# Performance work log

Hardware: AMD Instinct MI355X
Metric: run time of the kernel (lower is better)

The kernel has to match this reference:

```python
import jax, jax.numpy as jnp
import numpy as np

B, S, E, H = 2, 2048, 1024, 16
D = E // H  # head_dim = 64


def setup_inputs() -> dict:
    key = jax.random.key(0)
    ks = jax.random.split(key, 9)
    sc = 1.0 / np.sqrt(E)
    return {
        "x": jax.random.normal(ks[0], (B, S, E), dtype=jnp.float32),
        "Wq": jax.random.normal(ks[1], (E, E), dtype=jnp.float32) * sc,
        "bq": jnp.zeros((E,), dtype=jnp.float32),
        "Wk": jax.random.normal(ks[2], (E, E), dtype=jnp.float32) * sc,
        "bk": jnp.zeros((E,), dtype=jnp.float32),
        "Wv": jax.random.normal(ks[3], (E, E), dtype=jnp.float32) * sc,
        "bv": jnp.zeros((E,), dtype=jnp.float32),
        "Wo": jax.random.normal(ks[4], (E, E), dtype=jnp.float32) * sc,
        "bo": jnp.zeros((E,), dtype=jnp.float32),
    }


def reference(x, Wq, bq, Wk, bk, Wv, bv, Wo, bo):
    b, s, e = x.shape
    # projections: [B,S,E] -> [B,H,S,D]
    def heads(w, bias):
        return (x @ w + bias).reshape(b, s, H, D).transpose(0, 2, 1, 3)
    q, k, v = heads(Wq, bq), heads(Wk, bk), heads(Wv, bv)
    # scores [B,H,S,S]
    scores = jnp.einsum("bhqd,bhkd->bhqk", q, k) / jnp.sqrt(jnp.float32(D))
    causal = jnp.tril(jnp.ones((s, s), dtype=bool))
    scores = jnp.where(causal[None, None], scores, -jnp.inf)
    weights = jax.nn.softmax(scores, axis=-1)
    out = jnp.einsum("bhqk,bhkd->bhqd", weights, v)
    out = out.transpose(0, 2, 1, 3).reshape(b, s, e)
    return out @ Wo + bo
```

## Files before the change

kernel.cpp:

```cpp
#include <hip/hip_runtime.h>
#include <hip/hip_bf16.h>

#define B_SZ 2
#define S_LEN 2048
#define E_DIM 1024
#define NH 16
#define DH 64
#define M_ROWS (B_SZ * S_LEN)
#define QB 128
#define KVB 64

typedef __attribute__((ext_vector_type(8))) short short8;
typedef __attribute__((ext_vector_type(4))) float floatx4;

static __device__ __forceinline__ unsigned short f2bf(float f) {
    __hip_bfloat16 h = __float2bfloat16(f);
    return *reinterpret_cast<unsigned short*>(&h);
}
static __device__ __forceinline__ float bf2f(unsigned short u) {
    unsigned int v = ((unsigned int)u) << 16;
    return __builtin_bit_cast(float, v);
}

static __device__ __forceinline__ void gl2lds16(const void* g, void* l) {
    __builtin_amdgcn_global_load_lds((const __attribute__((address_space(1))) void*)g,
                                     (__attribute__((address_space(3))) void*)l, 16, 0, 0);
}

#define WAIT_VM0() asm volatile("s_waitcnt vmcnt(0)" ::: "memory")
#define WAIT_LGKM0() asm volatile("s_waitcnt lgkmcnt(0)" ::: "memory")

__global__ __launch_bounds__(256) void prep(const float* __restrict__ x,
                                            unsigned short* __restrict__ Xb,
                                            const float* __restrict__ W0,
                                            const float* __restrict__ W1,
                                            const float* __restrict__ W2,
                                            const float* __restrict__ W3,
                                            unsigned short* __restrict__ T0,
                                            unsigned short* __restrict__ T1,
                                            unsigned short* __restrict__ T2,
                                            unsigned short* __restrict__ T3) {
    __shared__ float tile[32][33];
    int bid = blockIdx.x;
    int t = threadIdx.x;
    if (bid < 4096) {
        int i = (bid * 256 + t) * 4;
        float4 v = *reinterpret_cast<const float4*>(x + i);
        ushort4 o;
        o.x = f2bf(v.x); o.y = f2bf(v.y); o.z = f2bf(v.z); o.w = f2bf(v.w);
        *reinterpret_cast<ushort4*>(Xb + i) = o;
        return;
    }
    int u = bid - 4096;
    int z = u >> 10, rest = u & 1023;
    int bx = (rest & 31) * 32, by = (rest >> 5) * 32;
    const float* W = (z == 0) ? W0 : (z == 1) ? W1 : (z == 2) ? W2 : W3;
    unsigned short* Wt = (z == 0) ? T0 : (z == 1) ? T1 : (z == 2) ? T2 : T3;
    int tx = t & 31, ty = t >> 5;
#pragma unroll
    for (int i = 0; i < 32; i += 8)
        tile[ty + i][tx] = W[(size_t)(by + ty + i) * E_DIM + bx + tx];
    __syncthreads();
#pragma unroll
    for (int i = 0; i < 32; i += 8)
        Wt[(size_t)(bx + ty + i) * E_DIM + by + tx] = f2bf(tile[tx][ty + i]);
}

#define QSCALE 0.18033688011112042f

__global__ __launch_bounds__(512, 2) void gemm_qkv8(const unsigned short* __restrict__ Wcat,
                                                    const unsigned short* __restrict__ Xb,
                                                    const float* __restrict__ bq,
                                                    const float* __restrict__ bk,
                                                    const float* __restrict__ bv,
                                                    unsigned short* __restrict__ Qg,
                                                    unsigned short* __restrict__ Kg,
                                                    unsigned short* __restrict__ Vtg) {
    __shared__ __align__(16) char lds[2][2][32768];

    int t = threadIdx.x;
    int b = blockIdx.x;
    int xcd = b & 7, ii = b >> 3;
    int it = (xcd & 3) * 3 + (ii >> 3);
    int jt = (xcd >> 2) * 8 + (ii & 7);
    int iBase = it << 8, jBase = jt << 8;

    int w = t >> 6, lane = t & 63;
    int lr = lane & 15, lh = lane >> 4;
    int wm = w >> 2, wn = w & 3;

    int srow = t >> 3;
    int scbx = ((t & 7) << 4) ^ ((srow & 7) << 4);

    const char* Ab = (const char*)Wcat;
    const char* Bb = (const char*)Xb;

    floatx4 acc[8][4];
#pragma unroll
    for (int i = 0; i < 8; i++)
#pragma unroll
        for (int j = 0; j < 4; j++) acc[i][j] = (floatx4){0.f, 0.f, 0.f, 0.f};

    auto stageA = [&](int buf, int kt) {
        int k0b = kt << 7;
#pragma unroll
        for (int c = 0; c < 4; c++)
            gl2lds16(Ab + (size_t)(iBase + c * 64 + srow) * 2048 + k0b + scbx,
                     &lds[buf][0][c * 8192 + t * 16]);
    };
    auto stageB = [&](int buf, int kt) {
        int k0b = kt << 7;
#pragma unroll
        for (int c = 0; c < 4; c++)
            gl2lds16(Bb + (size_t)(jBase + c * 64 + srow) * 2048 + k0b + scbx,
                     &lds[buf][1][c * 8192 + t * 16]);
    };

    short8 af[4][2], bf[4][2];
    auto rdA = [&](int buf, int qm) {
#pragma unroll
        for (int mi = 0; mi < 4; mi++)
#pragma unroll
            for (int ks = 0; ks < 2; ks++) {
                int row = wm * 128 + qm * 64 + mi * 16 + lr;
                af[mi][ks] = *reinterpret_cast<const short8*>(
                    &lds[buf][0][(row * 128 + ks * 64 + lh * 16) ^ ((row & 7) << 4)]);
            }
    };
    auto rdB = [&](int buf, int qn) {
#pragma unroll
        for (int ni = 0; ni < 2; ni++)
#pragma unroll
            for (int ks = 0; ks < 2; ks++) {
                int row = wn * 64 + qn * 32 + ni * 16 + lr;
                bf[qn * 2 + ni][ks] = *reinterpret_cast<const short8*>(
                    &lds[buf][1][(row * 128 + ks * 64 + lh * 16) ^ ((row & 7) << 4)]);
            }
    };
    auto mfma16 = [&](int qm, int qn) {
        __builtin_amdgcn_s_setprio(1);
#pragma unroll
        for (int mi = 0; mi < 4; mi++)
#pragma unroll
            for (int ni = 0; ni < 2; ni++)
#pragma unroll
                for (int ks = 0; ks < 2; ks++)
                    acc[qm * 4 + mi][qn * 2 + ni] = __builtin_amdgcn_mfma_f32_16x16x32_bf16(
                        af[mi][ks], bf[qn * 2 + ni][ks], acc[qm * 4 + mi][qn * 2 + ni], 0, 0, 0);
        __builtin_amdgcn_s_setprio(0);
    };

    const int NT = 16;
    stageA(0, 0);
    stageB(0, 0);
    WAIT_VM0();
    __builtin_amdgcn_s_barrier();

    for (int kt = 0; kt < NT; ++kt) {
        int cur = kt & 1, nxt = cur ^ 1;
        bool pf = (kt + 1 < NT);
        rdA(cur, 0);
        rdB(cur, 0);
        if (pf) stageA(nxt, kt + 1);
        __builtin_amdgcn_s_barrier();
        WAIT_LGKM0();
        __builtin_amdgcn_sched_barrier(0);
        mfma16(0, 0);
        __builtin_amdgcn_s_barrier();
        rdB(cur, 1);
        if (pf) stageB(nxt, kt + 1);
        __builtin_amdgcn_s_barrier();
        WAIT_LGKM0();
        __builtin_amdgcn_sched_barrier(0);
        mfma16(0, 1);
        __builtin_amdgcn_s_barrier();
        rdA(cur, 1);
        __builtin_amdgcn_s_barrier();
        WAIT_LGKM0();
        __builtin_amdgcn_sched_barrier(0);
        mfma16(1, 0);
        __builtin_amdgcn_s_barrier();
        if (pf) WAIT_VM0();
        __builtin_amdgcn_s_barrier();
        mfma16(1, 1);
        __builtin_amdgcn_s_barrier();
    }

    int wsel = iBase >> 10;
    const float* bias = (wsel == 0) ? bq : (wsel == 1) ? bk : bv;
    __syncthreads();

    if (wsel < 2) {
        unsigned short* O = wsel ? Kg : Qg;
        float scale = wsel ? 1.0f : QSCALE;
#pragma unroll
        for (int mi8 = 0; mi8 < 8; mi8++) {
            int i = iBase + wm * 128 + mi8 * 16 + lh * 4;
            int im = i & 1023;
            int h = im >> 6, d0 = im & 63;
            float4 bs = *reinterpret_cast<const float4*>(&bias[im]);
#pragma unroll
            for (int nf = 0; nf < 4; nf++) {
                int j = jBase + wn * 64 + nf * 16 + lr;
                int b_ = j >> 11, s = j & (S_LEN - 1);
                ushort4 pk;
                pk.x = f2bf((acc[mi8][nf][0] + bs.x) * scale);
                pk.y = f2bf((acc[mi8][nf][1] + bs.y) * scale);
                pk.z = f2bf((acc[mi8][nf][2] + bs.z) * scale);
                pk.w = f2bf((acc[mi8][nf][3] + bs.w) * scale);
                *reinterpret_cast<ushort4*>(
                    &O[((size_t)(b_ * NH + h) * S_LEN + s) * DH + d0]) = pk;
            }
        }
    } else {
        char* lw = &lds[0][0][0] + w * 16384;
#pragma unroll
        for (int mi8 = 0; mi8 < 8; mi8++) {
            int i = iBase + wm * 128 + mi8 * 16 + lh * 4;
            float4 bs = *reinterpret_cast<const float4*>(&bias[i & 1023]);
#pragma unroll
            for (int nf = 0; nf < 4; nf++) {
                int jl = nf * 16 + lr;
#pragma unroll
                for (int r = 0; r < 4; r++) {
                    int il = mi8 * 16 + lh * 4 + r;
                    float bb = (r == 0) ? bs.x : (r == 1) ? bs.y : (r == 2) ? bs.z : bs.w;
                    *reinterpret_cast<unsigned short*>(
                        lw + ((il * 128 + jl * 2) ^ ((il & 7) << 4))) =
                        f2bf(acc[mi8][nf][r] + bb);
                }
            }
        }
        __syncthreads();
#pragma unroll
        for (int rep = 0; rep < 16; rep++) {
            int idx = rep * 64 + lane;
            int il = idx >> 3, jb = idx & 7;
            short8 vv = *reinterpret_cast<const short8*>(
                lw + ((il * 128 + jb * 16) ^ ((il & 7) << 4)));
            int i = iBase + wm * 128 + il;
            int im = i & 1023;
            int h = im >> 6, d = im & 63;
            int j = jBase + wn * 64 + jb * 8;
            int b_ = j >> 11, s = j & (S_LEN - 1);
            *reinterpret_cast<short8*>(
                &Vtg[((size_t)(b_ * NH + h) * DH + d) * S_LEN + s]) = vv;
        }
    }
}

template <int NI>
static __device__ __forceinline__ void gemm_tile_mainloop(
    const unsigned short* __restrict__ A, const unsigned short* __restrict__ Bt,
    int mBase, int nBase, char* ldsA, char* ldsB, floatx4 (&acc)[4][NI]) {
    const int K = E_DIM;
    int t = threadIdx.x;
    int w = t >> 6, lane = t & 63;
    int lr = lane & 15, lh = lane >> 4;
    int wm = w >> 1, wn = w & 1;
    const char* Ab = (const char*)A;
    const char* Bb = (const char*)Bt;
    int srow = t >> 3;
    int scb = ((t & 7) << 4) ^ ((srow & 7) << 4);

#pragma unroll
    for (int mi = 0; mi < 4; mi++)
#pragma unroll
        for (int ni = 0; ni < NI; ni++) acc[mi][ni] = (floatx4){0.f, 0.f, 0.f, 0.f};

    for (int kt = 0; kt < K / 64; ++kt) {
        int k0 = kt * 64;
#pragma unroll
        for (int i = 0; i < 4; i++)
            gl2lds16(Ab + (size_t)(mBase + i * 32 + srow) * (K * 2) + k0 * 2 + scb,
                     ldsA + i * 4096 + t * 16);
#pragma unroll
        for (int i = 0; i < NI; i++)
            gl2lds16(Bb + (size_t)(nBase + i * 32 + srow) * (K * 2) + k0 * 2 + scb,
                     ldsB + i * 4096 + t * 16);
        __syncthreads();
#pragma unroll
        for (int ks = 0; ks < 2; ks++) {
            short8 af[4], bfr[NI];
#pragma unroll
            for (int mi = 0; mi < 4; mi++) {
                int row = wm * 64 + mi * 16 + lr;
                af[mi] = *reinterpret_cast<const short8*>(
                    ldsA + ((row * 128 + ks * 64 + lh * 16) ^ ((row & 7) << 4)));
            }
#pragma unroll
            for (int ni = 0; ni < NI; ni++) {
                int row = wn * (NI * 16) + ni * 16 + lr;
                bfr[ni] = *reinterpret_cast<const short8*>(
                    ldsB + ((row * 128 + ks * 64 + lh * 16) ^ ((row & 7) << 4)));
            }
#pragma unroll
            for (int mi = 0; mi < 4; mi++)
#pragma unroll
                for (int ni = 0; ni < NI; ni++)
                    acc[mi][ni] = __builtin_amdgcn_mfma_f32_16x16x32_bf16(af[mi], bfr[ni],
                                                                          acc[mi][ni], 0, 0, 0);
        }
        __syncthreads();
    }
}

__global__ __launch_bounds__(256) void gemm_o(const unsigned short* __restrict__ Og,
                                              const unsigned short* __restrict__ Wot,
                                              const float* __restrict__ bo,
                                              float* __restrict__ out) {
    __shared__ __align__(16) char ldsA[16384];
    __shared__ __align__(16) char ldsB[8192];
    int bid = blockIdx.y * 16 + blockIdx.x;
    int xcd = bid & 7, ii = bid >> 3;
    int xx = ii & 15;
    int yy = (xcd << 2) | (ii >> 4);
    int nBase = xx << 6;
    int mBase = yy << 7;

    floatx4 acc[4][2];
    gemm_tile_mainloop<2>(Og, Wot, mBase, nBase, ldsA, ldsB, acc);

    int w = threadIdx.x >> 6, lane = threadIdx.x & 63;
    int lr = lane & 15, lh = lane >> 4;
    int wm = w >> 1, wn = w & 1;
#pragma unroll
    for (int mi = 0; mi < 4; mi++)
#pragma unroll
        for (int ni = 0; ni < 2; ni++)
#pragma unroll
            for (int r = 0; r < 4; r++) {
                int m = mBase + wm * 64 + mi * 16 + lh * 4 + r;
                int n = nBase + wn * 32 + ni * 16 + lr;
                out[(size_t)m * E_DIM + n] = acc[mi][ni][r] + bo[n];
            }
}

__global__ __launch_bounds__(256) void attn_fwd(const unsigned short* __restrict__ Qg,
                                                const unsigned short* __restrict__ Kg,
                                                const unsigned short* __restrict__ Vtg,
                                                unsigned short* __restrict__ Og,
                                                unsigned short* __restrict__ Opart,
                                                float* __restrict__ lpart) {
    __shared__ __align__(16) char kt_lds[2][KVB * 128];
    __shared__ __align__(16) char vt_lds[2][KVB * 128];
    __shared__ __align__(16) unsigned short p_lds[4][32][72];

    int bid = blockIdx.x;
    int xcd = bid & 7, ii = bid >> 3;
    int bh = (xcd << 2) + ii / 30;
    int jj = 29 - (ii % 30);
    int qb, ch, c;
    if (jj < 6)        { qb = jj; ch = 0; c = 1; }
    else if (jj < 18)  { int u = jj - 6;  qb = 6 + (u >> 1); ch = u & 1; c = 2; }
    else               { int u = jj - 18; qb = 12 + u / 3;   ch = u % 3; c = 3; }
    int T = 2 * qb + 2;
    int kt_lo = ch * T / c;
    int kt_hi = (ch + 1) * T / c - 1;
    bool split = (c > 1);

    int w = threadIdx.x >> 6, lane = threadIdx.x & 63;
    int lr = lane & 15, lh = lane >> 4;
    int q0 = qb * QB + w * 32;

    const char* Kb = (const char*)(Kg + (size_t)bh * S_LEN * DH);
    const char* Vb = (const char*)(Vtg + (size_t)bh * DH * S_LEN);
    const unsigned short* Qb = Qg + (size_t)bh * S_LEN * DH;

    int wi0 = w * 2;
    int srow0 = wi0 * 8 + (lane >> 3);
    int scol = (lane & 7) << 4;

    auto stage = [&](int buf, int kt) {
        int kv0 = kt * KVB;
#pragma unroll
        for (int i = 0; i < 2; ++i) {
            int row = srow0 + i * 8;
            int colb = scol ^ ((row & 7) << 4);
            gl2lds16(Kb + (size_t)(kv0 + row) * 128 + colb,
                     kt_lds[buf] + (wi0 + i) * 1024);
            gl2lds16(Vb + (size_t)row * (S_LEN * 2) + (size_t)kv0 * 2 + colb,
                     vt_lds[buf] + (wi0 + i) * 1024);
        }
    };

    short8 aq[2][2];
#pragma unroll
    for (int m = 0; m < 2; m++)
#pragma unroll
        for (int ks = 0; ks < 2; ks++)
            aq[m][ks] = *reinterpret_cast<const short8*>(
                Qb + (size_t)(q0 + m * 16 + lr) * DH + ks * 32 + lh * 8);

    floatx4 oacc[2][4];
    float lsum[2][4];
#pragma unroll
    for (int m = 0; m < 2; m++) {
#pragma unroll
        for (int dt = 0; dt < 4; dt++) oacc[m][dt] = (floatx4){0.f, 0.f, 0.f, 0.f};
#pragma unroll
        for (int r = 0; r < 4; r++) lsum[m][r] = 0.f;
    }

    stage(0, kt_lo);
    __syncthreads();
    int buf = 0;

    for (int kt = kt_lo; kt <= kt_hi; ++kt) {
        if (kt < kt_hi) stage(buf ^ 1, kt + 1);
        int kv0 = kt * KVB;
        bool skip = (kv0 > q0 + 31);
        if (!skip) {
            const char* Kt = kt_lds[buf];
            const char* Vt = vt_lds[buf];
            floatx4 sacc[2][4];
#pragma unroll
            for (int m = 0; m < 2; m++)
#pragma unroll
                for (int nt = 0; nt < 4; nt++) sacc[m][nt] = (floatx4){0.f, 0.f, 0.f, 0.f};
#pragma unroll
            for (int ks = 0; ks < 2; ks++)
#pragma unroll
                for (int nt = 0; nt < 4; nt++) {
                    int row = nt * 16 + lr;
                    int addr = (row * 128 + ks * 64 + lh * 16) ^ ((row & 7) << 4);
                    short8 bk = *reinterpret_cast<const short8*>(Kt + addr);
#pragma unroll
                    for (int m = 0; m < 2; m++)
                        sacc[m][nt] = __builtin_amdgcn_mfma_f32_16x16x32_bf16(
                            aq[m][ks], bk, sacc[m][nt], 0, 0, 0);
                }
            if (kv0 + KVB - 1 > q0) {
#pragma unroll
                for (int m = 0; m < 2; m++)
#pragma unroll
                    for (int nt = 0; nt < 4; nt++)
#pragma unroll
                        for (int r = 0; r < 4; r++) {
                            int qrow = q0 + m * 16 + lh * 4 + r;
                            int kcol = kv0 + nt * 16 + lr;
                            if (kcol > qrow) sacc[m][nt][r] = -1e30f;
                        }
            }
#pragma unroll
            for (int m = 0; m < 2; m++) {
                float rs[4] = {0.f, 0.f, 0.f, 0.f};
#pragma unroll
                for (int nt = 0; nt < 4; nt++)
#pragma unroll
                    for (int r = 0; r < 4; r++) {
                        float p = __builtin_amdgcn_exp2f(sacc[m][nt][r]);
                        rs[r] += p;
                        p_lds[w][m * 16 + lh * 4 + r][nt * 16 + lr] = f2bf(p);
                    }
#pragma unroll
                for (int r = 0; r < 4; r++) lsum[m][r] += rs[r];
            }
            WAIT_LGKM0();
            short8 pa[2][2];
#pragma unroll
            for (int m = 0; m < 2; m++)
#pragma unroll
                for (int ks = 0; ks < 2; ks++)
                    pa[m][ks] = *reinterpret_cast<const short8*>(
                        &p_lds[w][m * 16 + lr][ks * 32 + lh * 8]);
#pragma unroll
            for (int ks = 0; ks < 2; ks++)
#pragma unroll
                for (int dt = 0; dt < 4; dt++) {
                    int row = dt * 16 + lr;
                    int addr = (row * 128 + ks * 64 + lh * 16) ^ ((row & 7) << 4);
                    short8 bv = *reinterpret_cast<const short8*>(Vt + addr);
#pragma unroll
                    for (int m = 0; m < 2; m++)
                        oacc[m][dt] = __builtin_amdgcn_mfma_f32_16x16x32_bf16(
                            pa[m][ks], bv, oacc[m][dt], 0, 0, 0);
                }
        }
        __syncthreads();
        buf ^= 1;
    }

#pragma unroll
    for (int m = 0; m < 2; m++)
#pragma unroll
        for (int msk = 1; msk < 16; msk <<= 1)
#pragma unroll
            for (int r = 0; r < 4; r++) lsum[m][r] += __shfl_xor(lsum[m][r], msk);

    if (split) {
        int base = (qb < 12) ? (qb - 6) * 2 : 12 + (qb - 12) * 3;
        int pi = bh * 24 + base + ch;
        unsigned short* Op = Opart + (size_t)pi * (QB * DH);
        float* lp = lpart + (size_t)pi * QB;
#pragma unroll
        for (int m = 0; m < 2; m++) {
#pragma unroll
            for (int r = 0; r < 4; r++) {
                int row = w * 32 + m * 16 + lh * 4 + r;
#pragma unroll
                for (int dt = 0; dt < 4; dt++)
                    Op[row * DH + dt * 16 + lr] = f2bf(oacc[m][dt][r]);
                if (lr == r) lp[row] = lsum[m][r];
            }
        }
    } else {
        int b_ = bh >> 4, h_ = bh & 15;
#pragma unroll
        for (int m = 0; m < 2; m++)
#pragma unroll
            for (int r = 0; r < 4; r++) {
                float inv = 1.f / lsum[m][r];
                int srow = q0 + m * 16 + lh * 4 + r;
#pragma unroll
                for (int dt = 0; dt < 4; dt++)
                    Og[((size_t)b_ * S_LEN + srow) * E_DIM + h_ * 64 + dt * 16 + lr] =
                        f2bf(oacc[m][dt][r] * inv);
            }
    }
}

__global__ __launch_bounds__(256) void attn_reduce(const unsigned short* __restrict__ Opart,
                                                   const float* __restrict__ lpart,
                                                   unsigned short* __restrict__ Og) {
    int bh = blockIdx.x;
    int qb = 6 + blockIdx.y;
    int c = (qb < 12) ? 2 : 3;
    int base = (qb < 12) ? (qb - 6) * 2 : 12 + (qb - 12) * 3;
    int pi0 = bh * 24 + base;
    const unsigned short* P0 = Opart + (size_t)pi0 * (QB * DH);
    const float* l0 = lpart + (size_t)pi0 * QB;
    int t = threadIdx.x;
    int cg = t & 7, r0 = t >> 3;
    int b_ = bh >> 4, h_ = bh & 15;
    int qrow0 = qb * QB;
#pragma unroll
    for (int rr = 0; rr < 4; rr++) {
        int row = r0 + rr * 32;
        float ls = l0[row] + l0[QB + row];
        if (c == 3) ls += l0[2 * QB + row];
        float inv = 1.f / ls;
        short8 v0 = *reinterpret_cast<const short8*>(P0 + row * DH + cg * 8);
        short8 v1 = *reinterpret_cast<const short8*>(P0 + QB * DH + row * DH + cg * 8);
        float s[8];
#pragma unroll
        for (int j = 0; j < 8; j++)
            s[j] = bf2f((unsigned short)v0[j]) + bf2f((unsigned short)v1[j]);
        if (c == 3) {
            short8 v2 = *reinterpret_cast<const short8*>(P0 + 2 * QB * DH + row * DH + cg * 8);
#pragma unroll
            for (int j = 0; j < 8; j++) s[j] += bf2f((unsigned short)v2[j]);
        }
        short8 o;
#pragma unroll
        for (int j = 0; j < 8; j++) o[j] = (short)f2bf(s[j] * inv);
        *reinterpret_cast<short8*>(Og + ((size_t)b_ * S_LEN + qrow0 + row) * E_DIM +
                                   h_ * 64 + cg * 8) = o;
    }
}

extern "C" void kernel_launch(void* const* d_in, const int* in_sizes, int n_in,
                              void* d_out, int out_size, void* d_ws, size_t ws_size,
                              hipStream_t stream) {
    const float* x  = (const float*)d_in[0];
    const float* Wq = (const float*)d_in[1];
    const float* bq = (const float*)d_in[2];
    const float* Wk = (const float*)d_in[3];
    const float* bk = (const float*)d_in[4];
    const float* Wv = (const float*)d_in[5];
    const float* bv = (const float*)d_in[6];
    const float* Wo = (const float*)d_in[7];
    const float* bo = (const float*)d_in[8];
    float* out = (float*)d_out;

    const size_t NX = (size_t)M_ROWS * E_DIM;
    const size_t NW = (size_t)E_DIM * E_DIM;
    unsigned short* ws  = (unsigned short*)d_ws;
    unsigned short* Xb  = ws;
    unsigned short* Wqt = Xb + NX;
    unsigned short* Wkt = Wqt + NW;
    unsigned short* Wvt = Wkt + NW;
    unsigned short* Wot = Wvt + NW;
    unsigned short* Qg  = Wot + NW;
    unsigned short* Kg  = Qg + NX;
    unsigned short* Vtg = Kg + NX;
    unsigned short* Og  = Vtg + NX;
    unsigned short* Opart = Xb;
    float* lpart = (float*)(Opart + (size_t)32 * 24 * QB * DH);

    prep<<<dim3(8192), 256, 0, stream>>>(x, Xb, Wq, Wk, Wv, Wo, Wqt, Wkt, Wvt, Wot);

    gemm_qkv8<<<dim3(192), 512, 0, stream>>>(Wqt, Xb, bq, bk, bv, Qg, Kg, Vtg);

    attn_fwd<<<dim3(960), 256, 0, stream>>>(Qg, Kg, Vtg, Og, Opart, lpart);
    attn_reduce<<<dim3(B_SZ * NH, 10), 256, 0, stream>>>(Opart, lpart, Og);

    gemm_o<<<dim3(E_DIM / 64, M_ROWS / 128), 256, 0, stream>>>(Og, Wot, bo, out);
}
```

Before: 119.1 us.

## Compute transposed scores and pass P via lane shuffles instead of LDS

Measured after the change: 113.6 us. -4.7%, faster.

```diff
diff --git a/kernel.cpp b/kernel.cpp
--- a/kernel.cpp
+++ b/kernel.cpp
@@ -12,6 +12,7 @@
 
 typedef __attribute__((ext_vector_type(8))) short short8;
 typedef __attribute__((ext_vector_type(4))) float floatx4;
+typedef __attribute__((ext_vector_type(4))) int intx4;
 
 static __device__ __forceinline__ unsigned short f2bf(float f) {
     __hip_bfloat16 h = __float2bfloat16(f);
@@ -20,6 +21,9 @@
 static __device__ __forceinline__ float bf2f(unsigned short u) {
     unsigned int v = ((unsigned int)u) << 16;
     return __builtin_bit_cast(float, v);
+}
+static __device__ __forceinline__ unsigned int pack2bf(float lo, float hi) {
+    return (unsigned int)f2bf(lo) | ((unsigned int)f2bf(hi) << 16);
 }
 
 static __device__ __forceinline__ void gl2lds16(const void* g, void* l) {
@@ -336,15 +340,14 @@
             }
 }
 
-__global__ __launch_bounds__(256) void attn_fwd(const unsigned short* __restrict__ Qg,
-                                                const unsigned short* __restrict__ Kg,
-                                                const unsigned short* __restrict__ Vtg,
-                                                unsigned short* __restrict__ Og,
-                                                unsigned short* __restrict__ Opart,
-                                                float* __restrict__ lpart) {
+__global__ __launch_bounds__(256, 4) void attn_fwd(const unsigned short* __restrict__ Qg,
+                                                   const unsigned short* __restrict__ Kg,
+                                                   const unsigned short* __restrict__ Vtg,
+                                                   unsigned short* __restrict__ Og,
+                                                   unsigned short* __restrict__ Opart,
+                                                   float* __restrict__ lpart) {
     __shared__ __align__(16) char kt_lds[2][KVB * 128];
     __shared__ __align__(16) char vt_lds[2][KVB * 128];
-    __shared__ __align__(16) unsigned short p_lds[4][32][72];
 
     int bid = blockIdx.x;
     int xcd = bid & 7, ii = bid >> 3;
@@ -393,13 +396,12 @@
                 Qb + (size_t)(q0 + m * 16 + lr) * DH + ks * 32 + lh * 8);
 
     floatx4 oacc[2][4];
-    float lsum[2][4];
+    float lsum[2];
 #pragma unroll
     for (int m = 0; m < 2; m++) {
 #pragma unroll
         for (int dt = 0; dt < 4; dt++) oacc[m][dt] = (floatx4){0.f, 0.f, 0.f, 0.f};
-#pragma unroll
-        for (int r = 0; r < 4; r++) lsum[m][r] = 0.f;
+        lsum[m] = 0.f;
     }
 
     stage(0, kt_lo);
@@ -428,7 +430,7 @@
 #pragma unroll
                     for (int m = 0; m < 2; m++)
                         sacc[m][nt] = __builtin_amdgcn_mfma_f32_16x16x32_bf16(
-                            aq[m][ks], bk, sacc[m][nt], 0, 0, 0);
+                            bk, aq[m][ks], sacc[m][nt], 0, 0, 0);
                 }
             if (kv0 + KVB - 1 > q0) {
 #pragma unroll
@@ -437,33 +439,44 @@
                     for (int nt = 0; nt < 4; nt++)
 #pragma unroll
                         for (int r = 0; r < 4; r++) {
-                            int qrow = q0 + m * 16 + lh * 4 + r;
-                            int kcol = kv0 + nt * 16 + lr;
+                            int kcol = kv0 + nt * 16 + lh * 4 + r;
+                            int qrow = q0 + m * 16 + lr;
                             if (kcol > qrow) sacc[m][nt][r] = -1e30f;
                         }
             }
+            unsigned int pk[2][4][2];
 #pragma unroll
             for (int m = 0; m < 2; m++) {
-                float rs[4] = {0.f, 0.f, 0.f, 0.f};
-#pragma unroll
-                for (int nt = 0; nt < 4; nt++)
+                float ls = 0.f;
+#pragma unroll
+                for (int nt = 0; nt < 4; nt++) {
 #pragma unroll
                     for (int r = 0; r < 4; r++) {
                         float p = __builtin_amdgcn_exp2f(sacc[m][nt][r]);
-                        rs[r] += p;
-                        p_lds[w][m * 16 + lh * 4 + r][nt * 16 + lr] = f2bf(p);
+                        sacc[m][nt][r] = p;
+                        ls += p;
                     }
-#pragma unroll
-                for (int r = 0; r < 4; r++) lsum[m][r] += rs[r];
-            }
-            WAIT_LGKM0();
+                    pk[m][nt][0] = pack2bf(sacc[m][nt][0], sacc[m][nt][1]);
+                    pk[m][nt][1] = pack2bf(sacc[m][nt][2], sacc[m][nt][3]);
+                }
+                lsum[m] += ls;
+            }
             short8 pa[2][2];
+            int hsel = lh >> 1;
 #pragma unroll
             for (int m = 0; m < 2; m++)
 #pragma unroll
-                for (int ks = 0; ks < 2; ks++)
-                    pa[m][ks] = *reinterpret_cast<const short8*>(
-                        &p_lds[w][m * 16 + lr][ks * 32 + lh * 8]);
+                for (int ks = 0; ks < 2; ks++) {
+                    intx4 u;
+#pragma unroll
+                    for (int t4 = 0; t4 < 4; t4++) {
+                        int src = lr + 32 * (lh & 1) + 16 * (t4 >> 1);
+                        int r0 = __shfl((int)pk[m][2 * ks][t4 & 1], src);
+                        int r1 = __shfl((int)pk[m][2 * ks + 1][t4 & 1], src);
+                        u[t4] = hsel ? r1 : r0;
+                    }
+                    pa[m][ks] = __builtin_bit_cast(short8, u);
+                }
 #pragma unroll
             for (int ks = 0; ks < 2; ks++)
 #pragma unroll
@@ -482,11 +495,10 @@
     }
 
 #pragma unroll
-    for (int m = 0; m < 2; m++)
-#pragma unroll
-        for (int msk = 1; msk < 16; msk <<= 1)
-#pragma unroll
-            for (int r = 0; r < 4; r++) lsum[m][r] += __shfl_xor(lsum[m][r], msk);
+    for (int m = 0; m < 2; m++) {
+        lsum[m] += __shfl_xor(lsum[m], 16);
+        lsum[m] += __shfl_xor(lsum[m], 32);
+    }
 
     if (split) {
         int base = (qb < 12) ? (qb - 6) * 2 : 12 + (qb - 12) * 3;
@@ -495,28 +507,30 @@
         float* lp = lpart + (size_t)pi * QB;
 #pragma unroll
         for (int m = 0; m < 2; m++) {
+            if (lh == 0) lp[w * 32 + m * 16 + lr] = lsum[m];
 #pragma unroll
             for (int r = 0; r < 4; r++) {
                 int row = w * 32 + m * 16 + lh * 4 + r;
 #pragma unroll
                 for (int dt = 0; dt < 4; dt++)
                     Op[row * DH + dt * 16 + lr] = f2bf(oacc[m][dt][r]);
-                if (lr == r) lp[row] = lsum[m][r];
             }
         }
     } else {
         int b_ = bh >> 4, h_ = bh & 15;
 #pragma unroll
-        for (int m = 0; m < 2; m++)
+        for (int m = 0; m < 2; m++) {
 #pragma unroll
             for (int r = 0; r < 4; r++) {
-                float inv = 1.f / lsum[m][r];
+                float lv = __shfl(lsum[m], lh * 4 + r);
+                float inv = 1.f / lv;
                 int srow = q0 + m * 16 + lh * 4 + r;
 #pragma unroll
                 for (int dt = 0; dt < 4; dt++)
                     Og[((size_t)b_ * S_LEN + srow) * E_DIM + h_ * 64 + dt * 16 + lr] =
                         f2bf(oacc[m][dt][r] * inv);
             }
+        }
     }
 }
 
```
